# Optimization experiments

Hardware: AMD Instinct MI355X
Metric: run time of the kernel (lower is better)

## Reference

```python
import jax, jax.numpy as jnp
import numpy as np

B, C, DET, T = 16, 1, 512, 180  # batch, channels, detector size (= image side, circle=True), n angles


def setup_inputs() -> dict:
    key = jax.random.key(0)
    x = jax.random.normal(key, (B, C, DET, T), dtype=jnp.float32)  # sinogram [B,C,det,theta]
    return {"x": x}


def _ramp_filter(x):
    """skimage-style ramp (Ram-Lak) filter along detector axis (axis=2)."""
    det = x.shape[2]
    size = max(64, int(2 ** np.ceil(np.log2(2 * det))))  # zero-padded FFT length
    n = np.concatenate([np.arange(1, size // 2 + 1, 2), np.arange(size // 2 - 1, 0, -2)])
    f = np.zeros(size, dtype=np.float64)
    f[0] = 0.25
    f[1::2] = -1.0 / (np.pi * n) ** 2
    fourier = (2.0 * np.real(np.fft.fft(f))).astype(np.float32)  # [size]
    xp = jnp.pad(x, ((0, 0), (0, 0), (0, size - det), (0, 0)))
    proj = jnp.fft.fft(xp, axis=2) * fourier[None, None, :, None]
    return jnp.real(jnp.fft.ifft(proj, axis=2))[:, :, :det, :].astype(x.dtype)


def _forward(x):
    b, c, det, n_theta = x.shape
    xf = _ramp_filter(x)
    # align_corners=False unit grid over the image (circle=True -> grid side == det)
    u = ((2.0 * jnp.arange(det, dtype=x.dtype) + 1.0) / det - 1.0)
    yg = u[:, None]  # [det,1] (meshgrid 'ij': Y varies over rows)
    xg = u[None, :]  # [1,det]
    rad = jnp.arange(n_theta, dtype=x.dtype) * jnp.asarray(np.pi / 180.0, x.dtype)
    cos_t, sin_t = jnp.cos(rad), jnp.sin(rad)

    # Note: the grid X coord theta_x[i]=(2i+1)/T-1 maps (align_corners=False) to pixel
    # index exactly i, so the width-axis bilinear interp reduces to taking angle column i.
    def body(reco, inp):
        i, c_, s_ = inp
        col = jax.lax.dynamic_index_in_dim(xf, i, axis=3, keepdims=False)  # [B,C,det]
        t = xg * c_ - yg * s_                      # [det,det] rotated coordinate
        iy = ((t + 1.0) * det - 1.0) / 2.0         # grid_sample align_corners=False
        i0f = jnp.floor(iy)
        w1 = iy - i0f
        w0 = 1.0 - w1
        i0 = i0f.astype(jnp.int32)
        i1 = i0 + 1
        m0 = ((i0 >= 0) & (i0 < det)).astype(xf.dtype)  # zeros padding
        m1 = ((i1 >= 0) & (i1 < det)).astype(xf.dtype)
        g0 = jnp.take(col, jnp.clip(i0, 0, det - 1), axis=2)  # [B,C,det,det]
        g1 = jnp.take(col, jnp.clip(i1, 0, det - 1), axis=2)
        return reco + (w0 * m0) * g0 + (w1 * m1) * g1, None

    reco0 = jnp.zeros((b, c, det, det), xf.dtype)
    reco, _ = jax.lax.scan(body, reco0, (jnp.arange(n_theta), cos_t, sin_t))

    # reconstruction circle mask (scikit=False -> radius^2 <= 1 - 1/in_size)
    mask = (xg ** 2 + yg ** 2) <= (1.0 - 1.0 / det)
    reco = jnp.where(mask[None, None], reco, jnp.zeros((), reco.dtype))
    return reco * jnp.asarray(np.pi / (2.0 * n_theta), reco.dtype)


def reference(x):
    return _forward(x)
```

## Files before the change

### kernel.cpp

```cpp
#include <hip/hip_runtime.h>
#include <math.h>

#define DET 512
#define NB  16
#define NT  180
#define PI_D 3.14159265358979323846
#define NPAIR 89
#define PADQ 108
#define NGP  45
#define NENT 768
#define ROWB 12288
#define NOFF 101
#define NMRG 6
#define NBX  108

#define TT_OFF   8192
#define XF0_OFF  (TT_OFF + 512*512*2)
#define XF90_OFF (XF0_OFF + 32768)
#define PK_OFF   (XF90_OFF + 32768)

typedef _Float16 half8  __attribute__((ext_vector_type(8)));
typedef _Float16 half4v __attribute__((ext_vector_type(4)));
typedef _Float16 half2v __attribute__((ext_vector_type(2)));
typedef float    float4v __attribute__((ext_vector_type(4)));

__device__ inline half2v H2(unsigned u) { half2v h; __builtin_memcpy(&h, &u, 4); return h; }
__device__ inline half2v pkrtz(float a, float b) {
  auto r = __builtin_amdgcn_cvt_pkrtz(a, b);
  half2v h; __builtin_memcpy(&h, &r, 4); return h;
}
__device__ inline float fdot2f(half2v a, half2v b, float c) {
  return __builtin_amdgcn_fdot2(a, b, c, false);
}
__device__ inline unsigned PK2(float a, float b) {
  half2v h; h.x = (_Float16)a; h.y = (_Float16)b;
  unsigned u; __builtin_memcpy(&u, &h, 4); return u;
}

__global__ __launch_bounds__(256) void filter_kernel(const float* __restrict__ x,
                                                     char* __restrict__ wsb) {
  __shared__ _Float16 xs_h[16][512];
  __shared__ _Float16 xs_l[16][512];
  __shared__ float xfs[16][65];
  __shared__ _Float16 wls[8][1032];
  char* pkb = wsb + PK_OFF;

  int tid = threadIdx.x;
  int p = blockIdx.x, b = blockIdx.y;
  int dt0 = blockIdx.z * 2;

  {
    int k0 = tid * 4;
    const float CSC = (float)(-2048.0 / (PI_D * PI_D));
#pragma unroll
    for (int r = 0; r < 8; r++) {
      half4v v;
#pragma unroll
      for (int j = 0; j < 4; j++) {
        int delta = 511 - (k0 + j) - r;
        float wv;
        if (delta == 0) wv = 512.0f;
        else if (delta & 1) wv = CSC / (float)(delta * delta);
        else wv = 0.0f;
        v[j] = (_Float16)wv;
      }
      *(half4v*)&wls[r][k0] = v;
    }
  }

  int m = tid & 15, kp = tid >> 4;
  int tS;
  if (p < 11) tS = (m < 8) ? (8 * p + 1 + m) : (164 - 8 * p + m);
  else        tS = (m == 0) ? 89 : ((m == 1) ? 91 : ((m == 3) ? 90 : 0));
  const float* xb = x + (size_t)b * DET * NT + tS;
#pragma unroll 8
  for (int pass = 0; pass < 16; pass++) {
    int k = pass * 32 + kp * 2;
    int c = k >> 3, h = k & 7;
    int phys = (((c ^ (m & 7)) << 3) | h);
    float v0 = xb[(size_t)k * NT];
    float v1 = xb[(size_t)(k + 1) * NT];
    _Float16 h0 = (_Float16)v0, h1 = (_Float16)v1;
    half2v hh = {h0, h1};
    half2v ll = {(_Float16)(v0 - (float)h0), (_Float16)(v1 - (float)h1)};
    *(half2v*)&xs_h[m][phys] = hh;
    *(half2v*)&xs_l[m][phys] = ll;
  }
  __syncthreads();

  int nprb = (p < 11) ? 8 : 1;
  int tpb0 = (p < 11) ? 8 * p : 88;
  if (blockIdx.z == 0) {
    for (int pr = 0; pr < nprb; pr++) {
      int tq = (p < 11) ? (tpb0 + pr) : 88;
      int gp = (tq <= 44) ? tq : 88 - tq;
      char* base = pkb + ((size_t)b * NGP + gp) * ROWB;
      if (tid < 107) {
        uint4 z4 = {0u, 0u, 0u, 0u};
        *(uint4*)(base + (size_t)tid * 16) = z4;
      } else if (tid < 255) {
        uint4 z4 = {0u, 0u, 0u, 0u};
        *(uint4*)(base + (size_t)(620 + tid - 107) * 16) = z4;
      } else {
        unsigned short z = 0;
        *(unsigned short*)(base + 107*16 + 0)  = z; *(unsigned short*)(base + 107*16 + 4)  = z;
        *(unsigned short*)(base + 107*16 + 8)  = z; *(unsigned short*)(base + 107*16 + 12) = z;
        *(unsigned short*)(base + 619*16 + 2)  = z; *(unsigned short*)(base + 619*16 + 6)  = z;
        *(unsigned short*)(base + 619*16 + 10) = z; *(unsigned short*)(base + 619*16 + 14) = z;
      }
    }
  }

  int lane = tid & 63, wv = tid >> 6;
  int mm = lane & 15, q = lane >> 4;
  const _Float16* arh = &xs_h[mm][0];
  const _Float16* arl = &xs_l[mm][0];
  int e = mm & 7;
  int mp = tid >> 5, cc = (tid & 31) * 2;
  int rT = (p < 11) ? mp : 0;
  int rU = (p < 11) ? (15 - mp) : 1;
  int tpp = (p < 11) ? (8 * p + mp) : 88;
  bool dopack = (p < 11) || (mp == 0);
  int gp_  = (tpp <= 44) ? tpp : 88 - tpp;
  int so   = (tpp <= 44) ? 0 : 8;

  for (int dti = 0; dti < 2; dti++) {
    int dt = dt0 + dti;
    int dw = dt * 64 + wv * 16 + mm;
    int sdw = 511 - dw;
    const _Float16* thl = &wls[sdw & 7][sdw & ~7];
    float4v acc0 = {0.f, 0.f, 0.f, 0.f};
    float4v acc1 = {0.f, 0.f, 0.f, 0.f};
#pragma unroll 4
    for (int kc = 0; kc < 512; kc += 32) {
      int ph = ((((kc >> 3) + q) ^ e) << 3);
      half8 Ah = *(const half8*)&arh[ph];
      half8 Al = *(const half8*)&arl[ph];
      half8 Bh = *(const half8*)&thl[kc + q * 8];
      acc0 = __builtin_amdgcn_mfma_f32_16x16x32_f16(Ah, Bh, acc0, 0, 0, 0);
      acc1 = __builtin_amdgcn_mfma_f32_16x16x32_f16(Al, Bh, acc1, 0, 0, 0);
    }
    if (dti > 0) __syncthreads();
#pragma unroll
    for (int i = 0; i < 4; i++)
      xfs[q * 4 + i][wv * 16 + mm] = (acc0[i] + acc1[i]) * 0.0009765625f;
    __syncthreads();
    if (dopack) {
      char* base = pkb + ((size_t)b * NGP + gp_) * ROWB;
      float ft0 = xfs[rT][cc], ft1 = xfs[rT][cc + 1];
      float fu0 = xfs[rU][cc], fu1 = xfs[rU][cc + 1];
      int en = PADQ + dt * 64 + cc;
      uint2 e0; e0.x = PK2(ft0, ft1); e0.y = PK2(fu0, fu1);
      *(uint2*)(base + (size_t)en * 16 + so) = e0;
      if (tpp == 44) *(uint2*)(base + (size_t)en * 16 + 8) = e0;
      if (cc < 62) {
        float ft2 = xfs[rT][cc + 2], fu2 = xfs[rU][cc + 2];
        uint2 e1; e1.x = PK2(ft1, ft2); e1.y = PK2(fu1, fu2);
        *(uint2*)(base + (size_t)(en + 1) * 16 + so) = e1;
        if (tpp == 44) *(uint2*)(base + (size_t)(en + 1) * 16 + 8) = e1;
      } else {
        _Float16 h1 = (_Float16)ft1, g1 = (_Float16)fu1;
        *(_Float16*)(base + (size_t)(en + 1) * 16 + 0 + so) = h1;
        *(_Float16*)(base + (size_t)(en + 1) * 16 + 4 + so) = g1;
        if (tpp == 44) {
          *(_Float16*)(base + (size_t)(en + 1) * 16 + 8)  = h1;
          *(_Float16*)(base + (size_t)(en + 1) * 16 + 12) = g1;
        }
      }
      if (cc == 0) {
        _Float16 h0 = (_Float16)ft0, g0 = (_Float16)fu0;
        *(_Float16*)(base + (size_t)(en - 1) * 16 + 2 + so) = h0;
        *(_Float16*)(base + (size_t)(en - 1) * 16 + 6 + so) = g0;
        if (tpp == 44) {
          *(_Float16*)(base + (size_t)(en - 1) * 16 + 10) = h0;
          *(_Float16*)(base + (size_t)(en - 1) * 16 + 14) = g0;
        }
      }
    }
    if (p == 11 && tid < 64) {
      float* f0  = (float*)(wsb + XF0_OFF)  + (size_t)b * DET;
      float* f90 = (float*)(wsb + XF90_OFF) + (size_t)b * DET;
      f0[dt * 64 + tid]  = xfs[2][tid];
      f90[dt * 64 + tid] = xfs[3][tid];
    }
  }
}

#define XTRACT(nm, qq, SW)                                                     \
  half2v Tft##nm = H2(SW ? qq.z : qq.x), Tfu##nm = H2(SW ? qq.w : qq.y);       \
  half2v Uft##nm = H2(SW ? qq.x : qq.z), Ufu##nm = H2(SW ? qq.y : qq.w);

#define PROCESS(c_, s_, SW)                                                    \
  {                                                                            \
    float inner = fmaf(-(s_), q_, 363.5f);                                     \
    float iyA = fmaf( (c_), p_, inner);                                        \
    float iyB = fmaf(-(c_), p_, inner);                                        \
    int   iA = (int)iyA;  float wA = __builtin_amdgcn_fractf(iyA);             \
    int   iB = (int)iyB;  float wB = __builtin_amdgcn_fractf(iyB);             \
    half2v wpA = pkrtz(1.f - wA, wA);                                          \
    half2v wpAr = pkrtz(wA, 1.f - wA);                                         \
    half2v wpB = pkrtz(1.f - wB, wB);                                          \
    half2v wpBr = pkrtz(wB, 1.f - wB);                                         \
    uint4 qA = colI[iA], qB = colI[iB];                                        \
    uint4 qMA = colI[726 - iA], qMB = colI[726 - iB];                          \
    XTRACT(A, qA, SW)  XTRACT(B, qB, SW)                                       \
    XTRACT(MA, qMA, SW) XTRACT(MB, qMB, SW)                                    \
    A1 = fdot2f(wpA, TftA, A1);   A1 = fdot2f(wpB, TfuB, A1);                  \
    A2 = fdot2f(wpB, TftB, A2);   A2 = fdot2f(wpA, TfuA, A2);                  \
    A3 = fdot2f(wpAr, TftMA, A3); A3 = fdot2f(wpBr, TfuMB, A3);                \
    A4 = fdot2f(wpBr, TftMB, A4); A4 = fdot2f(wpAr, TfuMA, A4);                \
    B1 = fdot2f(wpAr, UftMA, B1); B1 = fdot2f(wpB, UfuB, B1);                  \
    B2 = fdot2f(wpBr, UftMB, B2); B2 = fdot2f(wpA, UfuA, B2);                  \
    B3 = fdot2f(wpA, UftA, B3);   B3 = fdot2f(wpBr, UfuMB, B3);                \
    B4 = fdot2f(wpB, UftB, B4);   B4 = fdot2f(wpAr, UfuMA, B4);                \
  }

#define PROCESSP(c_, s_, SW, pp, qq_, AA1, AA2, AA3, AA4)                      \
  {                                                                            \
    float inner = fmaf(-(s_), (qq_), 363.5f);                                  \
    float iyA = fmaf( (c_), (pp), inner);                                      \
    float iyB = fmaf(-(c_), (pp), inner);                                      \
    int   iA = (int)iyA;  float wA = __builtin_amdgcn_fractf(iyA);             \
    int   iB = (int)iyB;  float wB = __builtin_amdgcn_fractf(iyB);             \
    half2v wpA = pkrtz(1.f - wA, wA);                                          \
    half2v wpAr = pkrtz(wA, 1.f - wA);                                         \
    half2v wpB = pkrtz(1.f - wB, wB);                                          \
    half2v wpBr = pkrtz(wB, 1.f - wB);                                         \
    uint4 qA = colI[iA], qB = colI[iB];                                        \
    uint4 qMA = colI[726 - iA], qMB = colI[726 - iB];                          \
    half2v TftA = H2(SW ? qA.z : qA.x),  TfuA = H2(SW ? qA.w : qA.y);          \
    half2v TftB = H2(SW ? qB.z : qB.x),  TfuB = H2(SW ? qB.w : qB.y);          \
    half2v TftMA = H2(SW ? qMA.z : qMA.x), TfuMA = H2(SW ? qMA.w : qMA.y);     \
    half2v TftMB = H2(SW ? qMB.z : qMB.x), TfuMB = H2(SW ? qMB.w : qMB.y);     \
    AA1 = fdot2f(wpA, TftA, AA1);   AA1 = fdot2f(wpB, TfuB, AA1);              \
    AA2 = fdot2f(wpB, TftB, AA2);   AA2 = fdot2f(wpA, TfuA, AA2);              \
    AA3 = fdot2f(wpAr, TftMA, AA3); AA3 = fdot2f(wpBr, TfuMB, AA3);            \
    AA4 = fdot2f(wpBr, TftMB, AA4); AA4 = fdot2f(wpAr, TfuMA, AA4);            \
  }

__global__ __launch_bounds__(256, 6) void backproj_kernel(
    const char* __restrict__ wsb, float* __restrict__ out) {
  __shared__ uint4 pk[2][NENT];
  __shared__ float2 trigs[48];
  int tid = threadIdx.x;
  int f = blockIdx.x;
  int sub = f & 15;
  int b = 2 * (sub & 7) + (sub >> 3);
  int bx = f >> 4;
  int lx = tid & 15, ly = tid >> 4;
  float* ob = out + (size_t)b * DET * DET;
  int w = tid >> 6, l = tid & 63;

  if (bx == NBX - 1) {
    const int LDEAD[10] = {10,8,6,5,4,3,2,2,1,1};
    for (int a = 0; a < 10; a++)
      for (int bt = 0; bt < LDEAD[a]; bt++) {
        int X1 = 16*a + lx, X2 = 511 - X1;
        int Y1 = 16*bt + ly, Y2 = 511 - Y1;
        ob[(size_t)Y1*DET + X1] = 0.f;
        ob[(size_t)Y1*DET + X2] = 0.f;
        ob[(size_t)Y2*DET + X1] = 0.f;
        ob[(size_t)Y2*DET + X2] = 0.f;
      }
    return;
  }

  if (tid < NGP) {
    float th = (float)(tid + 1) * (float)(PI_D / 180.0);
    float2 cs; cs.x = cosf(th); cs.y = sinf(th);
    trigs[tid] = cs;
  }

  const char* pkgb = wsb + PK_OFF + (size_t)b * NGP * ROWB;

  auto stage_group = [&](int g, int par) {
#pragma unroll
    for (int i = 0; i < 3; i++) {
      int c = w + 4 * i;
      const char* src = pkgb + (size_t)g * ROWB + c * 1024 + l * 16;
      char* dst = (char*)&pk[par][0] + c * 1024;
      __builtin_amdgcn_global_load_lds(
          (const __attribute__((address_space(1))) unsigned int*)src,
          (__attribute__((address_space(3))) unsigned int*)dst, 16, 0, 0);
    }
  };

  const float* f0  = (const float*)(wsb + XF0_OFF)  + (size_t)b * DET;
  const float* f90 = (const float*)(wsb + XF90_OFF) + (size_t)b * DET;
  const float SC = (float)(PI_D / 360.0);

  if (bx >= NOFF) {
    int d = bx - NOFF;
    int a1 = 4 + 2 * d, a2 = 5 + 2 * d;
    float p1_ = (float)(16 * a1 + lx) - 255.5f, q1_ = (float)(16 * a1 + ly) - 255.5f;
    float p2_ = (float)(16 * a2 + lx) - 255.5f, q2_ = (float)(16 * a2 + ly) - 255.5f;
    int mk1 = 481 - 32 * a1, mn1 = 505 - 32 * a1 - 8 * w;
    int mk2 = 481 - 32 * a2, mn2 = 505 - 32 * a2 - 8 * w;
    bool wl1 = (mk1 * mk1 + mn1 * mn1 <= 261632);
    bool wl2 = (mk2 * mk2 + mn2 * mn2 <= 261632);

    float A1=0.f, A2=0.f, A3=0.f, A4=0.f;
    float C1=0.f, C2=0.f, C3=0.f, C4=0.f;

    stage_group(0, 0);
    __syncthreads();
    for (int g = 0; g < NGP; g++) {
      if (g + 1 < NGP) stage_group(g + 1, (g + 1) & 1);
      float2 cs = trigs[g];
      const uint4* colI = &pk[g & 1][0];
      if (wl1) {
        PROCESSP(cs.x, cs.y, 0, p1_, q1_, A1, A2, A3, A4);
        if (g != 44) PROCESSP(cs.y, cs.x, 1, p1_, q1_, A1, A2, A3, A4);
      }
      if (wl2) {
        PROCESSP(cs.x, cs.y, 0, p2_, q2_, C1, C2, C3, C4);
        if (g != 44) PROCESSP(cs.y, cs.x, 1, p2_, q2_, C1, C2, C3, C4);
      }
      __syncthreads();
    }
#pragma unroll
    for (int t = 0; t < 2; t++) {
      int a = t ? a2 : a1;
      int X1 = 16 * a + lx, X2 = 511 - X1;
      int Y1 = 16 * a + ly, Y2 = 511 - Y1;
      int kx = 2 * X1 - 511, ky = 2 * Y1 - 511;
      bool in = (kx * kx + ky * ky) <= 261632;
      float g0x1 = f0[X1], g0x2 = f0[X2];
      float g90y1 = f90[Y1], g90y2 = f90[Y2];
      float P1 = (t ? C1 : A1) + g0x1 + g90y2;
      float P2 = (t ? C2 : A2) + g0x2 + g90y2;
      float P3 = (t ? C3 : A3) + g0x2 + g90y1;
      float P4 = (t ? C4 : A4) + g0x1 + g90y1;
      ob[(size_t)Y1 * DET + X1] = in ? P1 * SC : 0.f;
      ob[(size_t)Y1 * DET + X2] = in ? P2 * SC : 0.f;
      ob[(size_t)Y2 * DET + X2] = in ? P3 * SC : 0.f;
      ob[(size_t)Y2 * DET + X1] = in ? P4 * SC : 0.f;
    }
    return;
  }

  int a = (bx>=6)+(bx>=14)+(bx>=24)+(bx>=35)+(bx>=46)+(bx>=56)+(bx>=65)
        + (bx>=73)+(bx>=80)+(bx>=86)+(bx>=91)+(bx>=95)+(bx>=98)+(bx>=100);
  int Sa, bs;
  if (a < 8) { Sa = (int)((0x41382E23180E0600ULL >> (8*a)) & 0xFF);
               bs = (int)((0x080706050506080AULL >> (8*a)) & 0xFF); }
  else       { Sa = (int)((0x0064625F5B565049ULL >> (8*(a-8))) & 0xFF);
               bs = (int)((0x000F0E0D0C0B0A09ULL >> (8*(a-8))) & 0xFF); }
  int bt = bx - Sa + bs;
  int tx = 16*a, ty = 16*bt;

  int X1 = tx + lx, X2 = 511 - X1;
  int Y1 = ty + ly, Y2 = 511 - Y1;
  float p_ = (float)X1 - 255.5f;
  float q_ = (float)Y1 - 255.5f;

  int mkx = 481 - 32*a;
  int mky = 505 - 32*bt - 8*w;
  bool wlive = (mkx*mkx + mky*mky <= 261632);

  float A1=0.f, A2=0.f, A3=0.f, A4=0.f;
  float B1=0.f, B2=0.f, B3=0.f, B4=0.f;

  stage_group(0, 0);
  __syncthreads();

  for (int g = 0; g < NGP; g++) {
    if (g + 1 < NGP) stage_group(g + 1, (g + 1) & 1);
    float2 cs = trigs[g];
    const uint4* colI = &pk[g & 1][0];
    if (wlive) {
      PROCESS(cs.x, cs.y, 0);
      if (g != 44) PROCESS(cs.y, cs.x, 1);
    }
    __syncthreads();
  }

  int kx = 2*X1 - 511, ky = 2*Y1 - 511;
  bool in = (kx*kx + ky*ky) <= 261632;

  float g0x1 = f0[X1], g0x2 = f0[X2];
  float g90y1 = f90[Y1], g90y2 = f90[Y2];
  float P1 = A1 + g0x1 + g90y2;
  float P2 = A2 + g0x2 + g90y2;
  float P3 = A3 + g0x2 + g90y1;
  float P4 = A4 + g0x1 + g90y1;
  ob[(size_t)Y1*DET + X1] = in ? P1*SC : 0.f;
  ob[(size_t)Y1*DET + X2] = in ? P2*SC : 0.f;
  ob[(size_t)Y2*DET + X2] = in ? P3*SC : 0.f;
  ob[(size_t)Y2*DET + X1] = in ? P4*SC : 0.f;

  {
    float g0y1 = f0[Y1], g0y2 = f0[Y2];
    float g90x1 = f90[X1], g90x2 = f90[X2];
    float Q1 = B1 + g0y1 + g90x2;
    float Q2 = B2 + g0y1 + g90x1;
    float Q3 = B3 + g0y2 + g90x1;
    float Q4 = B4 + g0y2 + g90x2;
    Q1 = in ? Q1*SC : 0.f;
    Q2 = in ? Q2*SC : 0.f;
    Q3 = in ? Q3*SC : 0.f;
    Q4 = in ? Q4*SC : 0.f;
    __syncthreads();
    float* qs = (float*)&pk[0][0];
    qs[(0*16 + lx)*17 + ly] = Q1;
    qs[(1*16 + lx)*17 + ly] = Q2;
    qs[(2*16 + lx)*17 + ly] = Q3;
    qs[(3*16 + lx)*17 + ly] = Q4;
    __syncthreads();
    float o1 = qs[(0*16 + ly)*17 + lx];
    float o2 = qs[(1*16 + ly)*17 + lx];
    float o3 = qs[(2*16 + ly)*17 + lx];
    float o4 = qs[(3*16 + ly)*17 + lx];
    int r1 = tx + ly, r2 = 511 - r1;
    int c1 = ty + lx, c2 = 511 - c1;
    ob[(size_t)r1*DET + c1] = o1;
    ob[(size_t)r2*DET + c1] = o2;
    ob[(size_t)r2*DET + c2] = o3;
    ob[(size_t)r1*DET + c2] = o4;
  }
}

extern "C" void kernel_launch(void* const* d_in, const int* in_sizes, int n_in,
                              void* d_out, int out_size, void* d_ws, size_t ws_size,
                              hipStream_t stream) {
  (void)in_sizes; (void)n_in; (void)out_size; (void)ws_size;
  const float* x = (const float*)d_in[0];
  float* out = (float*)d_out;
  char*  wsb = (char*)d_ws;

  filter_kernel<<<dim3(12, 16, 4), 256, 0, stream>>>(x, wsb);
  backproj_kernel<<<dim3(NBX * NB), 256, 0, stream>>>(wsb, out);
}
```

Before: 140.1 us.

## Shrink packed projection rows by clamping indices instead of zero padding

Removes the wide zero-padded regions around each packed filtered projection row (768 to 516 entries). Out-of-range interpolation indices are now clamped onto zero sentinel entries at 3 and 515. This cuts global writes in the filter kernel, the global-to-LDS staging traffic and the LDS footprint in the backprojection kernel, and occupancy is raised from 6 to 8 blocks. The cost is two extra min/max per lookup. Clamping onto a single zero entry only approximates zero padding for indices just past the edge, which is valid only because the circle mask discards far-out samples.

```diff
diff --git a/kernel.cpp b/kernel.cpp
--- a/kernel.cpp
+++ b/kernel.cpp
@@ -6,10 +6,9 @@
 #define NT  180
 #define PI_D 3.14159265358979323846
 #define NPAIR 89
-#define PADQ 108
 #define NGP  45
-#define NENT 768
-#define ROWB 12288
+#define NENT 516
+#define ROWB 8256
 #define NOFF 101
 #define NMRG 6
 #define NBX  108
@@ -35,6 +34,9 @@
 __device__ inline unsigned PK2(float a, float b) {
   half2v h; h.x = (_Float16)a; h.y = (_Float16)b;
   unsigned u; __builtin_memcpy(&u, &h, 4); return u;
+}
+__device__ inline int clamp3_515(int i) {
+  return min(max(i, 3), 515);
 }
 
 __global__ __launch_bounds__(256) void filter_kernel(const float* __restrict__ x,
@@ -90,24 +92,16 @@
 
   int nprb = (p < 11) ? 8 : 1;
   int tpb0 = (p < 11) ? 8 * p : 88;
-  if (blockIdx.z == 0) {
+  if (blockIdx.z == 0 && tid == 0) {
     for (int pr = 0; pr < nprb; pr++) {
       int tq = (p < 11) ? (tpb0 + pr) : 88;
       int gp = (tq <= 44) ? tq : 88 - tq;
       char* base = pkb + ((size_t)b * NGP + gp) * ROWB;
-      if (tid < 107) {
-        uint4 z4 = {0u, 0u, 0u, 0u};
-        *(uint4*)(base + (size_t)tid * 16) = z4;
-      } else if (tid < 255) {
-        uint4 z4 = {0u, 0u, 0u, 0u};
-        *(uint4*)(base + (size_t)(620 + tid - 107) * 16) = z4;
-      } else {
-        unsigned short z = 0;
-        *(unsigned short*)(base + 107*16 + 0)  = z; *(unsigned short*)(base + 107*16 + 4)  = z;
-        *(unsigned short*)(base + 107*16 + 8)  = z; *(unsigned short*)(base + 107*16 + 12) = z;
-        *(unsigned short*)(base + 619*16 + 2)  = z; *(unsigned short*)(base + 619*16 + 6)  = z;
-        *(unsigned short*)(base + 619*16 + 10) = z; *(unsigned short*)(base + 619*16 + 14) = z;
-      }
+      unsigned short z = 0;
+      *(unsigned short*)(base + 3*16 + 0)  = z; *(unsigned short*)(base + 3*16 + 4)  = z;
+      *(unsigned short*)(base + 3*16 + 8)  = z; *(unsigned short*)(base + 3*16 + 12) = z;
+      *(unsigned short*)(base + 515*16 + 2)  = z; *(unsigned short*)(base + 515*16 + 6)  = z;
+      *(unsigned short*)(base + 515*16 + 10) = z; *(unsigned short*)(base + 515*16 + 14) = z;
     }
   }
 
@@ -149,7 +143,7 @@
       char* base = pkb + ((size_t)b * NGP + gp_) * ROWB;
       float ft0 = xfs[rT][cc], ft1 = xfs[rT][cc + 1];
       float fu0 = xfs[rU][cc], fu1 = xfs[rU][cc + 1];
-      int en = PADQ + dt * 64 + cc;
+      int en = 4 + dt * 64 + cc;
       uint2 e0; e0.x = PK2(ft0, ft1); e0.y = PK2(fu0, fu1);
       *(uint2*)(base + (size_t)en * 16 + so) = e0;
       if (tpp == 44) *(uint2*)(base + (size_t)en * 16 + 8) = e0;
@@ -192,17 +186,17 @@
 
 #define PROCESS(c_, s_, SW)                                                    \
   {                                                                            \
-    float inner = fmaf(-(s_), q_, 363.5f);                                     \
+    float inner = fmaf(-(s_), q_, 259.5f);                                     \
     float iyA = fmaf( (c_), p_, inner);                                        \
     float iyB = fmaf(-(c_), p_, inner);                                        \
-    int   iA = (int)iyA;  float wA = __builtin_amdgcn_fractf(iyA);             \
-    int   iB = (int)iyB;  float wB = __builtin_amdgcn_fractf(iyB);             \
+    int   iA = clamp3_515((int)iyA);  float wA = __builtin_amdgcn_fractf(iyA); \
+    int   iB = clamp3_515((int)iyB);  float wB = __builtin_amdgcn_fractf(iyB); \
     half2v wpA = pkrtz(1.f - wA, wA);                                          \
     half2v wpAr = pkrtz(wA, 1.f - wA);                                         \
     half2v wpB = pkrtz(1.f - wB, wB);                                          \
     half2v wpBr = pkrtz(wB, 1.f - wB);                                         \
     uint4 qA = colI[iA], qB = colI[iB];                                        \
-    uint4 qMA = colI[726 - iA], qMB = colI[726 - iB];                          \
+    uint4 qMA = colI[518 - iA], qMB = colI[518 - iB];                          \
     XTRACT(A, qA, SW)  XTRACT(B, qB, SW)                                       \
     XTRACT(MA, qMA, SW) XTRACT(MB, qMB, SW)                                    \
     A1 = fdot2f(wpA, TftA, A1);   A1 = fdot2f(wpB, TfuB, A1);                  \
@@ -217,17 +211,17 @@
 
 #define PROCESSP(c_, s_, SW, pp, qq_, AA1, AA2, AA3, AA4)                      \
   {                                                                            \
-    float inner = fmaf(-(s_), (qq_), 363.5f);                                  \
+    float inner = fmaf(-(s_), (qq_), 259.5f);                                  \
     float iyA = fmaf( (c_), (pp), inner);                                      \
     float iyB = fmaf(-(c_), (pp), inner);                                      \
-    int   iA = (int)iyA;  float wA = __builtin_amdgcn_fractf(iyA);             \
-    int   iB = (int)iyB;  float wB = __builtin_amdgcn_fractf(iyB);             \
+    int   iA = clamp3_515((int)iyA);  float wA = __builtin_amdgcn_fractf(iyA); \
+    int   iB = clamp3_515((int)iyB);  float wB = __builtin_amdgcn_fractf(iyB); \
     half2v wpA = pkrtz(1.f - wA, wA);                                          \
     half2v wpAr = pkrtz(wA, 1.f - wA);                                         \
     half2v wpB = pkrtz(1.f - wB, wB);                                          \
     half2v wpBr = pkrtz(wB, 1.f - wB);                                         \
     uint4 qA = colI[iA], qB = colI[iB];                                        \
-    uint4 qMA = colI[726 - iA], qMB = colI[726 - iB];                          \
+    uint4 qMA = colI[518 - iA], qMB = colI[518 - iB];                          \
     half2v TftA = H2(SW ? qA.z : qA.x),  TfuA = H2(SW ? qA.w : qA.y);          \
     half2v TftB = H2(SW ? qB.z : qB.x),  TfuB = H2(SW ? qB.w : qB.y);          \
     half2v TftMA = H2(SW ? qMA.z : qMA.x), TfuMA = H2(SW ? qMA.w : qMA.y);     \
@@ -238,7 +232,7 @@
     AA4 = fdot2f(wpBr, TftMB, AA4); AA4 = fdot2f(wpAr, TfuMA, AA4);            \
   }
 
-__global__ __launch_bounds__(256, 6) void backproj_kernel(
+__global__ __launch_bounds__(256, 8) void backproj_kernel(
     const char* __restrict__ wsb, float* __restrict__ out) {
   __shared__ uint4 pk[2][NENT];
   __shared__ float2 trigs[48];
@@ -274,14 +268,19 @@
   const char* pkgb = wsb + PK_OFF + (size_t)b * NGP * ROWB;
 
   auto stage_group = [&](int g, int par) {
+    const char* src = pkgb + (size_t)g * ROWB;
+    char* dst = (char*)&pk[par][0];
 #pragma unroll
-    for (int i = 0; i < 3; i++) {
+    for (int i = 0; i < 2; i++) {
       int c = w + 4 * i;
-      const char* src = pkgb + (size_t)g * ROWB + c * 1024 + l * 16;
-      char* dst = (char*)&pk[par][0] + c * 1024;
       __builtin_amdgcn_global_load_lds(
-          (const __attribute__((address_space(1))) unsigned int*)src,
-          (__attribute__((address_space(3))) unsigned int*)dst, 16, 0, 0);
+          (const __attribute__((address_space(1))) unsigned int*)(src + c * 1024 + l * 16),
+          (__attribute__((address_space(3))) unsigned int*)(dst + c * 1024),
+          16, 0, 0);
+    }
+    if (tid < 4) {
+      uint4 v = *(const uint4*)(src + 8192 + tid * 16);
+      *(uint4*)(dst + 8192 + tid * 16) = v;
     }
   };
 
```

After: 137.3 us. -2.0%, faster.
